# Kernel optimization log

Measured on AMD Instinct MI355X. Metric: run time of the kernel, lower is better.

The kernel has to match this reference:

```python
import jax, jax.numpy as jnp
import numpy as np

BLOCK_SIZE = 1024
OUTLIER_SIGMA = 3.0
OUT_FEATURES = 11008
IN_FEATURES = 4096
TOKENS = 64


def _quantize_mixed_np(W):
    """Faithful numpy port of quantize_mixed (BLOCK_SIZE divides numel exactly here)."""
    flat = W.astype(np.float32).reshape(-1)
    nb = flat.size // BLOCK_SIZE
    blocks = flat.reshape(nb, BLOCK_SIZE)
    mu = blocks.mean(axis=1, keepdims=True)
    sig = np.maximum(blocks.std(axis=1, ddof=1, keepdims=True), 1e-8)  # torch.std is unbiased
    outlier = np.abs(blocks - mu) > OUTLIER_SIGMA * sig
    abs_max = np.maximum(np.abs(np.where(outlier, 0.0, blocks)).max(axis=1), 1e-8)
    scales = (abs_max / 127.0).astype(np.float16)
    q = np.clip(np.round(blocks / abs_max[:, None] * 127.0), -127, 127).astype(np.int8)
    all_pos = np.arange(nb, dtype=np.int64)[:, None] * BLOCK_SIZE + np.arange(BLOCK_SIZE, dtype=np.int64)[None, :]
    int8_data = q[~outlier]                      # row-major == torch order
    fp16_data = blocks[outlier].astype(np.float16)
    int8_pos = all_pos[~outlier].astype(np.int32)
    fp16_pos = all_pos[outlier].astype(np.int32)
    block_idx = np.nonzero(~outlier)[0].astype(np.int32)  # block index per int8 value
    return int8_data, fp16_data, scales, int8_pos, fp16_pos, block_idx


def setup_inputs() -> dict:
    key = jax.random.key(0)
    k_x, k_b = jax.random.split(key)
    rng = np.random.default_rng(0)
    W = (rng.standard_normal((OUT_FEATURES, IN_FEATURES)) * 0.02).astype(np.float32)
    int8_data, fp16_data, scales, int8_pos, fp16_pos, block_idx = _quantize_mixed_np(W)
    x = jax.random.normal(k_x, (TOKENS, IN_FEATURES), dtype=jnp.float16)
    bias = jax.random.normal(k_b, (OUT_FEATURES,), dtype=jnp.float16) * jnp.float16(0.02)
    return {
        "x": x,
        "int8_data": jnp.asarray(int8_data),
        "fp16_data": jnp.asarray(fp16_data),
        "scales": jnp.asarray(scales),
        "bias": bias,
        "int8_pos": jnp.asarray(int8_pos),
        "fp16_pos": jnp.asarray(fp16_pos),
        "block_idx": jnp.asarray(block_idx),
    }


def reference(x, int8_data, fp16_data, scales, bias, int8_pos, fp16_pos, block_idx):
    out_features = bias.shape[0]
    in_features = x.shape[1]
    numel = out_features * in_features  # divisible by BLOCK_SIZE for these dims
    # dequantize_mixed: scatter fp16 outliers and dequantized int8 values into flat fp16 buffer
    flat = jnp.zeros((numel,), dtype=jnp.float16)
    flat = flat.at[fp16_pos].set(fp16_data)
    flat = flat.at[int8_pos].set(int8_data.astype(jnp.float16) * scales[block_idx])
    W = flat.reshape(out_features, in_features)
    # F.linear(x, W, bias) in fp16
    return jnp.dot(x.astype(jnp.float16), W.T) + bias
```

## Files before the change

### kernel.cpp

```cpp
#include <hip/hip_runtime.h>
#include <hip/hip_fp16.h>

#define TOK   64
#define INF   4096
#define OUTF  11008
#define NUMEL (OUTF * INF)
#define NSLC  (NUMEL / 64)
#define NBLK  (OUTF / 16)
#define KSPL  4
#define OUTN  (TOK * OUTF)

typedef __attribute__((ext_vector_type(8))) _Float16 half8;
typedef __attribute__((ext_vector_type(4))) _Float16 half4;
typedef __attribute__((ext_vector_type(4))) float floatx4;
typedef __attribute__((ext_vector_type(4), aligned(4))) int int4u;
typedef __attribute__((ext_vector_type(4))) int int4a;

__global__ __launch_bounds__(256) void precompute_kernel(
    const float* __restrict__ x, const int* __restrict__ fppos, int nf,
    _Float16* __restrict__ x16, int* __restrict__ meta) {
  const int t = blockIdx.x * 256 + threadIdx.x;
  if (t < (TOK * INF) / 4) {
    const floatx4 f = *(const floatx4*)&x[t * 4];
    half4 h;
    h[0] = (_Float16)f[0]; h[1] = (_Float16)f[1];
    h[2] = (_Float16)f[2]; h[3] = (_Float16)f[3];
    *(half4*)&x16[t * 4] = h;
  }
  if (t < NSLC) {
    const int target = t << 6;
    int lo = 0, hi = nf;
    while (lo < hi) {
      const int mid = (lo + hi) >> 1;
      if (fppos[mid] < target) lo = mid + 1; else hi = mid;
    }
    unsigned long long mask = 0ull;
    int j = lo;
    while (j < nf) {
      const int d = fppos[j] - target;
      if (d >= 64) break;
      mask |= 1ull << d;
      ++j;
    }
    int4a mv;
    mv[0] = lo;
    mv[1] = (int)(unsigned)(mask & 0xffffffffu);
    mv[2] = (int)(unsigned)(mask >> 32);
    mv[3] = 0;
    *(int4a*)&meta[t * 4] = mv;
  }
}

__device__ __forceinline__ void meta_window1(const int p0, const int4a mv,
                                             int& i0, unsigned& m8) {
  const unsigned mlo = (unsigned)mv[1];
  const unsigned mhi = (unsigned)mv[2];
  const int off = p0 & 63;
  m8 = 0xffu & (off < 32 ? (mlo >> off) : (mhi >> (off - 32)));
  const unsigned bl = (off >= 32) ? mlo : (mlo & ((1u << off) - 1u));
  const unsigned bh = (off >= 32) ? (mhi & ((1u << (off - 32)) - 1u)) : 0u;
  i0 = p0 - mv[0] - (__popc(bl) + __popc(bh));
}

__device__ __forceinline__ half8 finish_slot(
    const unsigned m8, const int i0, const int p0, const float s,
    const int (&l)[8], const int* __restrict__ i8,
    const float* __restrict__ fpdat, const int n8) {
  const int f = (int)m8;
  float ov[8];
#pragma unroll
  for (int e = 0; e < 8; ++e) ov[e] = 0.f;
  if (f) {
    int fi = p0 - i0;
#pragma unroll
    for (int e = 0; e < 8; ++e) {
      if ((f >> e) & 1) { ov[e] = fpdat[fi]; ++fi; }
    }
  }

  half8 oh;
  if (i0 + 8 <= n8) {
    if (f == 0) {
#pragma unroll
      for (int e = 0; e < 8; ++e) oh[e] = (_Float16)((float)l[e] * s);
    } else {
      int q = 0;
#pragma unroll
      for (int e = 0; e < 8; ++e) {
        const int flg = (f >> e) & 1;
        int lv = l[0];
#pragma unroll
        for (int qq = 1; qq < 8; ++qq) lv = (q == qq) ? l[qq] : lv;
        oh[e] = flg ? (_Float16)ov[e] : (_Float16)((float)lv * s);
        q += 1 - flg;
      }
    }
  } else {
    int c = 0;
    const int m = n8 - 1;
#pragma unroll
    for (int e = 0; e < 8; ++e) {
      const int flg = (f >> e) & 1;
      int idx = i0 + e - c;
      idx = idx < 0 ? 0 : (idx > m ? m : idx);
      oh[e] = flg ? (_Float16)ov[e] : (_Float16)((float)i8[idx] * s);
      c += flg;
    }
  }
  return oh;
}

struct Pre {
  int la[8], lb[8];
  int i0a, i0b;
  unsigned m8a, m8b;
  float va0, va1, vb0, vb1;
  half8 A[8];
};

__global__ __launch_bounds__(256, 3) void gemm_fused(
    const _Float16* __restrict__ x16, const int* __restrict__ i8,
    const float* __restrict__ fpdat, const float* __restrict__ scales,
    const int* __restrict__ meta, float* __restrict__ part,
    const int n8, const int nf) {
  __shared__ float red[4 * 64 * 16];

  const int tid  = threadIdx.x;
  const int wave = tid >> 6;
  const int lane = tid & 63;
  const int quad = lane >> 4;
  const int ln   = lane & 15;
  const int nt   = blockIdx.x >> 2;
  const int kq   = blockIdx.x & 3;
  const int n0   = nt << 4;
  const int kbas = kq * 1024 + wave * 256;
  const int qoff = quad * 8;

  const int prow  = n0 + ln;
  const int pbase = prow * INF + kbas;
  const float s   = scales[prow * 4 + kq];

#define ISSUE(BNK, CC, MV)                                                   \
  do {                                                                       \
    const int p0a_ = pbase + (CC) * 64 + qoff;                               \
    meta_window1(p0a_, (MV), BNK.i0a, BNK.m8a);                              \
    meta_window1(p0a_ + 32, (MV), BNK.i0b, BNK.m8b);                         \
    if (BNK.i0a + 8 <= n8) {                                                 \
      *(int4u*)&BNK.la[0] = *(const int4u*)&i8[BNK.i0a];                     \
      *(int4u*)&BNK.la[4] = *(const int4u*)&i8[BNK.i0a + 4];                 \
    }                                                                        \
    if (BNK.i0b + 8 <= n8) {                                                 \
      *(int4u*)&BNK.lb[0] = *(const int4u*)&i8[BNK.i0b];                     \
      *(int4u*)&BNK.lb[4] = *(const int4u*)&i8[BNK.i0b + 4];                 \
    }                                                                        \
    if (BNK.m8a) {                                                           \
      const int fia_ = p0a_ - BNK.i0a;                                       \
      BNK.va0 = fpdat[fia_];                                                 \
      BNK.va1 = fpdat[fia_ + 1 < nf ? fia_ + 1 : nf - 1];                    \
    }                                                                        \
    if (BNK.m8b) {                                                           \
      const int fib_ = p0a_ + 32 - BNK.i0b;                                  \
      BNK.vb0 = fpdat[fib_];                                                 \
      BNK.vb1 = fpdat[fib_ + 1 < nf ? fib_ + 1 : nf - 1];                    \
    }                                                                        \
    const _Float16* ap_ = &x16[ln * INF + kbas + (CC) * 64 + qoff];          \
    BNK.A[0] = *(const half8*)&ap_[0];                                       \
    BNK.A[1] = *(const half8*)&ap_[16 * INF];                                \
    BNK.A[2] = *(const half8*)&ap_[32 * INF];                                \
    BNK.A[3] = *(const half8*)&ap_[48 * INF];                                \
    BNK.A[4] = *(const half8*)&ap_[32];                                      \
    BNK.A[5] = *(const half8*)&ap_[16 * INF + 32];                           \
    BNK.A[6] = *(const half8*)&ap_[32 * INF + 32];                           \
    BNK.A[7] = *(const half8*)&ap_[48 * INF + 32];                           \
  } while (0)

#define FSLOT(OH, LARR, M8, I0, V0, V1)                                      \
  do {                                                                       \
    const int f_ = (int)(M8);                                                \
    if ((I0) + 8 <= n8) {                                                    \
      if (f_ == 0) {                                                         \
        _Pragma("unroll")                                                    \
        for (int e = 0; e < 8; ++e) OH[e] = (_Float16)((float)LARR[e] * s);  \
      } else {                                                               \
        int q_ = 0;                                                          \
        _Pragma("unroll")                                                    \
        for (int e = 0; e < 8; ++e) {                                        \
          const int flg = (f_ >> e) & 1;                                     \
          const int rank = __popc(f_ & ((1 << e) - 1));                      \
          const float fv = (rank == 0) ? (V0) : (V1);                        \
          int lv = LARR[0];                                                  \
          _Pragma("unroll")                                                  \
          for (int qq = 1; qq < 8; ++qq) lv = (q_ == qq) ? LARR[qq] : lv;    \
          OH[e] = flg ? (_Float16)fv : (_Float16)((float)lv * s);            \
          q_ += 1 - flg;                                                     \
        }                                                                    \
      }                                                                      \
    } else {                                                                 \
      int c_ = 0;                                                            \
      const int m_ = n8 - 1;                                                 \
      _Pragma("unroll")                                                      \
      for (int e = 0; e < 8; ++e) {                                          \
        const int flg = (f_ >> e) & 1;                                       \
        const int rank = __popc(f_ & ((1 << e) - 1));                        \
        const float fv = (rank == 0) ? (V0) : (V1);                          \
        int idx = (I0) + e - c_;                                             \
        idx = idx < 0 ? 0 : (idx > m_ ? m_ : idx);                           \
        OH[e] = flg ? (_Float16)fv : (_Float16)((float)i8[idx] * s);         \
        c_ += flg;                                                           \
      }                                                                      \
    }                                                                        \
  } while (0)

#define FIN_MFMA(BNK, CC)                                                    \
  do {                                                                       \
    const int p0a_ = pbase + (CC) * 64 + qoff;                               \
    half8 b0, b1;                                                            \
    FSLOT(b0, BNK.la, BNK.m8a, BNK.i0a, BNK.va0, BNK.va1);                   \
    FSLOT(b1, BNK.lb, BNK.m8b, BNK.i0b, BNK.vb0, BNK.vb1);                   \
    if (__any(__popc((int)BNK.m8a) > 2 || __popc((int)BNK.m8b) > 2)) {       \
      if (__popc((int)BNK.m8a) > 2)                                          \
        b0 = finish_slot(BNK.m8a, BNK.i0a, p0a_, s, BNK.la, i8, fpdat, n8);  \
      if (__popc((int)BNK.m8b) > 2)                                          \
        b1 = finish_slot(BNK.m8b, BNK.i0b, p0a_ + 32, s, BNK.lb,             \
                         i8, fpdat, n8);                                     \
    }                                                                        \
    acc0 = __builtin_amdgcn_mfma_f32_16x16x32_f16(BNK.A[0], b0, acc0, 0,0,0);\
    acc1 = __builtin_amdgcn_mfma_f32_16x16x32_f16(BNK.A[1], b0, acc1, 0,0,0);\
    acc2 = __builtin_amdgcn_mfma_f32_16x16x32_f16(BNK.A[2], b0, acc2, 0,0,0);\
    acc3 = __builtin_amdgcn_mfma_f32_16x16x32_f16(BNK.A[3], b0, acc3, 0,0,0);\
    acc0 = __builtin_amdgcn_mfma_f32_16x16x32_f16(BNK.A[4], b1, acc0, 0,0,0);\
    acc1 = __builtin_amdgcn_mfma_f32_16x16x32_f16(BNK.A[5], b1, acc1, 0,0,0);\
    acc2 = __builtin_amdgcn_mfma_f32_16x16x32_f16(BNK.A[6], b1, acc2, 0,0,0);\
    acc3 = __builtin_amdgcn_mfma_f32_16x16x32_f16(BNK.A[7], b1, acc3, 0,0,0);\
  } while (0)

  int4a mzA = *(const int4a*)&meta[(pbase >> 6) * 4];
  int4a mzB = *(const int4a*)&meta[((pbase + 64) >> 6) * 4];
  Pre pA, pB;
  ISSUE(pA, 0, mzA);

  floatx4 acc0 = {0,0,0,0}, acc1 = {0,0,0,0}, acc2 = {0,0,0,0}, acc3 = {0,0,0,0};

  ISSUE(pB, 1, mzB);
  mzA = *(const int4a*)&meta[((pbase + 128) >> 6) * 4];
  FIN_MFMA(pA, 0);
  ISSUE(pA, 2, mzA);
  mzB = *(const int4a*)&meta[((pbase + 192) >> 6) * 4];
  FIN_MFMA(pB, 1);
  ISSUE(pB, 3, mzB);
  FIN_MFMA(pA, 2);
  FIN_MFMA(pB, 3);

#undef ISSUE
#undef FSLOT
#undef FIN_MFMA

  const int mb = quad * 4;
#pragma unroll
  for (int i = 0; i < 4; ++i) red[wave * 1024 + (mb + i)      * 16 + ln] = acc0[i];
#pragma unroll
  for (int i = 0; i < 4; ++i) red[wave * 1024 + (16 + mb + i) * 16 + ln] = acc1[i];
#pragma unroll
  for (int i = 0; i < 4; ++i) red[wave * 1024 + (32 + mb + i) * 16 + ln] = acc2[i];
#pragma unroll
  for (int i = 0; i < 4; ++i) red[wave * 1024 + (48 + mb + i) * 16 + ln] = acc3[i];
  __syncthreads();

  float* pp = &part[(size_t)kq * OUTN];
#pragma unroll
  for (int c2 = 0; c2 < 4; ++c2) {
    const int cell = tid + c2 * 256;
    const int mm = cell >> 4, nn = cell & 15;
    pp[mm * OUTF + n0 + nn] =
        red[cell] + red[1024 + cell] + red[2048 + cell] + red[3072 + cell];
  }
}

__global__ __launch_bounds__(256) void reduce_kernel(
    const float* __restrict__ part, const float* __restrict__ bias,
    float* __restrict__ out) {
  const int t  = blockIdx.x * 256 + threadIdx.x;
  const int i4 = t * 4;
  floatx4 a = *(const floatx4*)&part[i4];
#pragma unroll
  for (int k = 1; k < KSPL; ++k) {
    const floatx4 b = *(const floatx4*)&part[(size_t)k * OUTN + i4];
    a[0] += b[0]; a[1] += b[1]; a[2] += b[2]; a[3] += b[3];
  }
  const int nn = i4 % OUTF;
  const floatx4 bb = *(const floatx4*)&bias[nn];
  a[0] += bb[0]; a[1] += bb[1]; a[2] += bb[2]; a[3] += bb[3];
  *(floatx4*)&out[i4] = a;
}

extern "C" void kernel_launch(void* const* d_in, const int* in_sizes, int n_in,
                              void* d_out, int out_size, void* d_ws,
                              size_t ws_size, hipStream_t stream) {
  const float* x      = (const float*)d_in[0];
  const int*   i8     = (const int*)d_in[1];
  const float* fpdat  = (const float*)d_in[2];
  const float* scales = (const float*)d_in[3];
  const float* bias   = (const float*)d_in[4];
  const int*   fppos  = (const int*)d_in[6];

  char* wsp = (char*)d_ws;
  _Float16* x16  = (_Float16*)wsp;
  int*      meta = (int*)(wsp + (size_t)TOK * INF * sizeof(_Float16));
  float*    part = (float*)(wsp + (size_t)TOK * INF * sizeof(_Float16)
                                + (size_t)NSLC * 16);
  float*    out  = (float*)d_out;

  const int n8 = in_sizes[1];
  const int nf = in_sizes[2];

  precompute_kernel<<<NSLC / 256, 256, 0, stream>>>(x, fppos, nf, x16, meta);
  gemm_fused<<<NBLK * KSPL, 256, 0, stream>>>(x16, i8, fpdat, scales, meta,
                                              part, n8, nf);
  reduce_kernel<<<OUTN / (4 * 256), 256, 0, stream>>>(part, bias, out);
}
```

Measured before the change: 438.3 us.

## Seed outlier binary search per chunk and load A fragments just-in-time

A new small kernel binary-searches the outlier position list once per 4096-element chunk. The precompute kernel then narrows each per-slice search to that chunk's range, which cuts global-memory search steps. The GEMM kernel stops prefetching the eight A fragments into the double-buffered Pre struct and loads them inside each stage instead. This lowers register pressure so launch bounds can rise from 3 to 4 blocks per SM, at the cost of less latency hiding for the A loads and one extra kernel launch.

```diff
diff --git a/kernel.cpp b/kernel.cpp
--- a/kernel.cpp
+++ b/kernel.cpp
@@ -6,6 +6,7 @@
 #define OUTF  11008
 #define NUMEL (OUTF * INF)
 #define NSLC  (NUMEL / 64)
+#define NSEED (NSLC / 64)
 #define NBLK  (OUTF / 16)
 #define KSPL  4
 #define OUTN  (TOK * OUTF)
@@ -16,9 +17,24 @@
 typedef __attribute__((ext_vector_type(4), aligned(4))) int int4u;
 typedef __attribute__((ext_vector_type(4))) int int4a;
 
+__global__ __launch_bounds__(256) void seed_kernel(
+    const int* __restrict__ fppos, int nf, int* __restrict__ seed) {
+  const int j = blockIdx.x * 256 + threadIdx.x;
+  if (j <= NSEED) {
+    const int target = j * 4096;
+    int lo = 0, hi = nf;
+    while (lo < hi) {
+      const int mid = (lo + hi) >> 1;
+      if (fppos[mid] < target) lo = mid + 1; else hi = mid;
+    }
+    seed[j] = lo;
+  }
+}
+
 __global__ __launch_bounds__(256) void precompute_kernel(
     const float* __restrict__ x, const int* __restrict__ fppos, int nf,
-    _Float16* __restrict__ x16, int* __restrict__ meta) {
+    const int* __restrict__ seed, _Float16* __restrict__ x16,
+    int* __restrict__ meta) {
   const int t = blockIdx.x * 256 + threadIdx.x;
   if (t < (TOK * INF) / 4) {
     const floatx4 f = *(const floatx4*)&x[t * 4];
@@ -29,7 +45,7 @@
   }
   if (t < NSLC) {
     const int target = t << 6;
-    int lo = 0, hi = nf;
+    int lo = seed[t >> 6], hi = seed[(t >> 6) + 1];
     while (lo < hi) {
       const int mid = (lo + hi) >> 1;
       if (fppos[mid] < target) lo = mid + 1; else hi = mid;
@@ -115,10 +131,9 @@
   int i0a, i0b;
   unsigned m8a, m8b;
   float va0, va1, vb0, vb1;
-  half8 A[8];
 };
 
-__global__ __launch_bounds__(256, 3) void gemm_fused(
+__global__ __launch_bounds__(256, 4) void gemm_fused(
     const _Float16* __restrict__ x16, const int* __restrict__ i8,
     const float* __restrict__ fpdat, const float* __restrict__ scales,
     const int* __restrict__ meta, float* __restrict__ part,
@@ -163,15 +178,6 @@
       BNK.vb0 = fpdat[fib_];                                                 \
       BNK.vb1 = fpdat[fib_ + 1 < nf ? fib_ + 1 : nf - 1];                    \
     }                                                                        \
-    const _Float16* ap_ = &x16[ln * INF + kbas + (CC) * 64 + qoff];          \
-    BNK.A[0] = *(const half8*)&ap_[0];                                       \
-    BNK.A[1] = *(const half8*)&ap_[16 * INF];                                \
-    BNK.A[2] = *(const half8*)&ap_[32 * INF];                                \
-    BNK.A[3] = *(const half8*)&ap_[48 * INF];                                \
-    BNK.A[4] = *(const half8*)&ap_[32];                                      \
-    BNK.A[5] = *(const half8*)&ap_[16 * INF + 32];                           \
-    BNK.A[6] = *(const half8*)&ap_[32 * INF + 32];                           \
-    BNK.A[7] = *(const half8*)&ap_[48 * INF + 32];                           \
   } while (0)
 
 #define FSLOT(OH, LARR, M8, I0, V0, V1)                                      \
@@ -211,6 +217,17 @@
     }                                                                        \
   } while (0)
 
+#define LOADA(CC)                                                            \
+  const _Float16* ap_ = &x16[ln * INF + kbas + (CC) * 64 + qoff];            \
+  const half8 A0 = *(const half8*)&ap_[0];                                   \
+  const half8 A1 = *(const half8*)&ap_[16 * INF];                            \
+  const half8 A2 = *(const half8*)&ap_[32 * INF];                            \
+  const half8 A3 = *(const half8*)&ap_[48 * INF];                            \
+  const half8 A4 = *(const half8*)&ap_[32];                                  \
+  const half8 A5 = *(const half8*)&ap_[16 * INF + 32];                       \
+  const half8 A6 = *(const half8*)&ap_[32 * INF + 32];                       \
+  const half8 A7 = *(const half8*)&ap_[48 * INF + 32]
+
 #define FIN_MFMA(BNK, CC)                                                    \
   do {                                                                       \
     const int p0a_ = pbase + (CC) * 64 + qoff;                               \
@@ -224,14 +241,14 @@
         b1 = finish_slot(BNK.m8b, BNK.i0b, p0a_ + 32, s, BNK.lb,             \
                          i8, fpdat, n8);                                     \
     }                                                                        \
-    acc0 = __builtin_amdgcn_mfma_f32_16x16x32_f16(BNK.A[0], b0, acc0, 0,0,0);\
-    acc1 = __builtin_amdgcn_mfma_f32_16x16x32_f16(BNK.A[1], b0, acc1, 0,0,0);\
-    acc2 = __builtin_amdgcn_mfma_f32_16x16x32_f16(BNK.A[2], b0, acc2, 0,0,0);\
-    acc3 = __builtin_amdgcn_mfma_f32_16x16x32_f16(BNK.A[3], b0, acc3, 0,0,0);\
-    acc0 = __builtin_amdgcn_mfma_f32_16x16x32_f16(BNK.A[4], b1, acc0, 0,0,0);\
-    acc1 = __builtin_amdgcn_mfma_f32_16x16x32_f16(BNK.A[5], b1, acc1, 0,0,0);\
-    acc2 = __builtin_amdgcn_mfma_f32_16x16x32_f16(BNK.A[6], b1, acc2, 0,0,0);\
-    acc3 = __builtin_amdgcn_mfma_f32_16x16x32_f16(BNK.A[7], b1, acc3, 0,0,0);\
+    acc0 = __builtin_amdgcn_mfma_f32_16x16x32_f16(A0, b0, acc0, 0, 0, 0);    \
+    acc1 = __builtin_amdgcn_mfma_f32_16x16x32_f16(A1, b0, acc1, 0, 0, 0);    \
+    acc2 = __builtin_amdgcn_mfma_f32_16x16x32_f16(A2, b0, acc2, 0, 0, 0);    \
+    acc3 = __builtin_amdgcn_mfma_f32_16x16x32_f16(A3, b0, acc3, 0, 0, 0);    \
+    acc0 = __builtin_amdgcn_mfma_f32_16x16x32_f16(A4, b1, acc0, 0, 0, 0);    \
+    acc1 = __builtin_amdgcn_mfma_f32_16x16x32_f16(A5, b1, acc1, 0, 0, 0);    \
+    acc2 = __builtin_amdgcn_mfma_f32_16x16x32_f16(A6, b1, acc2, 0, 0, 0);    \
+    acc3 = __builtin_amdgcn_mfma_f32_16x16x32_f16(A7, b1, acc3, 0, 0, 0);    \
   } while (0)
 
   int4a mzA = *(const int4a*)&meta[(pbase >> 6) * 4];
@@ -241,18 +258,31 @@
 
   floatx4 acc0 = {0,0,0,0}, acc1 = {0,0,0,0}, acc2 = {0,0,0,0}, acc3 = {0,0,0,0};
 
-  ISSUE(pB, 1, mzB);
-  mzA = *(const int4a*)&meta[((pbase + 128) >> 6) * 4];
-  FIN_MFMA(pA, 0);
-  ISSUE(pA, 2, mzA);
-  mzB = *(const int4a*)&meta[((pbase + 192) >> 6) * 4];
-  FIN_MFMA(pB, 1);
-  ISSUE(pB, 3, mzB);
-  FIN_MFMA(pA, 2);
-  FIN_MFMA(pB, 3);
+  {
+    LOADA(0);
+    ISSUE(pB, 1, mzB);
+    mzA = *(const int4a*)&meta[((pbase + 128) >> 6) * 4];
+    FIN_MFMA(pA, 0);
+  }
+  {
+    LOADA(1);
+    ISSUE(pA, 2, mzA);
+    mzB = *(const int4a*)&meta[((pbase + 192) >> 6) * 4];
+    FIN_MFMA(pB, 1);
+  }
+  {
+    LOADA(2);
+    ISSUE(pB, 3, mzB);
+    FIN_MFMA(pA, 2);
+  }
+  {
+    LOADA(3);
+    FIN_MFMA(pB, 3);
+  }
 
 #undef ISSUE
 #undef FSLOT
+#undef LOADA
 #undef FIN_MFMA
 
   const int mb = quad * 4;
@@ -308,12 +338,17 @@
   int*      meta = (int*)(wsp + (size_t)TOK * INF * sizeof(_Float16));
   float*    part = (float*)(wsp + (size_t)TOK * INF * sizeof(_Float16)
                                 + (size_t)NSLC * 16);
+  int*      seed = (int*)(wsp + (size_t)TOK * INF * sizeof(_Float16)
+                              + (size_t)NSLC * 16
+                              + (size_t)KSPL * OUTN * sizeof(float));
   float*    out  = (float*)d_out;
 
   const int n8 = in_sizes[1];
   const int nf = in_sizes[2];
 
-  precompute_kernel<<<NSLC / 256, 256, 0, stream>>>(x, fppos, nf, x16, meta);
+  seed_kernel<<<(NSEED + 256) / 256 + 1, 256, 0, stream>>>(fppos, nf, seed);
+  precompute_kernel<<<NSLC / 256, 256, 0, stream>>>(x, fppos, nf, seed,
+                                                    x16, meta);
   gemm_fused<<<NBLK * KSPL, 256, 0, stream>>>(x16, i8, fpdat, scales, meta,
                                               part, n8, nf);
   reduce_kernel<<<OUTN / (4 * 256), 256, 0, stream>>>(part, bias, out);
```

Measured after the change: 452.7 us. 1.03x slower.

## Split K eight ways, halve per-wave work, and drop A prefetch buffers

Applied to the files above, without the earlier changes.

Raises the K split from 4 to 8, so each wave handles 128 K elements (2 chunks) instead of 256, and the grid doubles in size. The per-bank A registers are replaced by one shared set loaded just before each MFMA group, and the outlier fp32 loads become unconditional with clamped indices. Launch bounds rise to 4 blocks per SIMD to lift occupancy. The aim is more parallelism and lower register pressure. In exchange, partial-sum traffic and the reduction work double, and A-load latency is exposed before the MFMAs with less overlap.

```diff
diff --git a/kernel.cpp b/kernel.cpp
--- a/kernel.cpp
+++ b/kernel.cpp
@@ -7,7 +7,7 @@
 #define NUMEL (OUTF * INF)
 #define NSLC  (NUMEL / 64)
 #define NBLK  (OUTF / 16)
-#define KSPL  4
+#define KSPL  8
 #define OUTN  (TOK * OUTF)
 
 typedef __attribute__((ext_vector_type(8))) _Float16 half8;
@@ -115,10 +115,9 @@
   int i0a, i0b;
   unsigned m8a, m8b;
   float va0, va1, vb0, vb1;
-  half8 A[8];
 };
 
-__global__ __launch_bounds__(256, 3) void gemm_fused(
+__global__ __launch_bounds__(256, 4) void gemm_fused(
     const _Float16* __restrict__ x16, const int* __restrict__ i8,
     const float* __restrict__ fpdat, const float* __restrict__ scales,
     const int* __restrict__ meta, float* __restrict__ part,
@@ -130,15 +129,15 @@
   const int lane = tid & 63;
   const int quad = lane >> 4;
   const int ln   = lane & 15;
-  const int nt   = blockIdx.x >> 2;
-  const int kq   = blockIdx.x & 3;
+  const int nt   = blockIdx.x >> 3;
+  const int kq   = blockIdx.x & 7;
   const int n0   = nt << 4;
-  const int kbas = kq * 1024 + wave * 256;
+  const int kbas = kq * 512 + wave * 128;
   const int qoff = quad * 8;
 
   const int prow  = n0 + ln;
   const int pbase = prow * INF + kbas;
-  const float s   = scales[prow * 4 + kq];
+  const float s   = scales[prow * 4 + (kq >> 1)];
 
 #define ISSUE(BNK, CC, MV)                                                   \
   do {                                                                       \
@@ -153,25 +152,17 @@
       *(int4u*)&BNK.lb[0] = *(const int4u*)&i8[BNK.i0b];                     \
       *(int4u*)&BNK.lb[4] = *(const int4u*)&i8[BNK.i0b + 4];                 \
     }                                                                        \
-    if (BNK.m8a) {                                                           \
-      const int fia_ = p0a_ - BNK.i0a;                                       \
+      \
+    {                                                                        \
+      int fia_ = p0a_ - BNK.i0a;                                             \
+      fia_ = fia_ < nf - 1 ? fia_ : nf - 1;                                  \
       BNK.va0 = fpdat[fia_];                                                 \
       BNK.va1 = fpdat[fia_ + 1 < nf ? fia_ + 1 : nf - 1];                    \
-    }                                                                        \
-    if (BNK.m8b) {                                                           \
-      const int fib_ = p0a_ + 32 - BNK.i0b;                                  \
+      int fib_ = p0a_ + 32 - BNK.i0b;                                        \
+      fib_ = fib_ < nf - 1 ? fib_ : nf - 1;                                  \
       BNK.vb0 = fpdat[fib_];                                                 \
       BNK.vb1 = fpdat[fib_ + 1 < nf ? fib_ + 1 : nf - 1];                    \
     }                                                                        \
-    const _Float16* ap_ = &x16[ln * INF + kbas + (CC) * 64 + qoff];          \
-    BNK.A[0] = *(const half8*)&ap_[0];                                       \
-    BNK.A[1] = *(const half8*)&ap_[16 * INF];                                \
-    BNK.A[2] = *(const half8*)&ap_[32 * INF];                                \
-    BNK.A[3] = *(const half8*)&ap_[48 * INF];                                \
-    BNK.A[4] = *(const half8*)&ap_[32];                                      \
-    BNK.A[5] = *(const half8*)&ap_[16 * INF + 32];                           \
-    BNK.A[6] = *(const half8*)&ap_[32 * INF + 32];                           \
-    BNK.A[7] = *(const half8*)&ap_[48 * INF + 32];                           \
   } while (0)
 
 #define FSLOT(OH, LARR, M8, I0, V0, V1)                                      \
@@ -211,6 +202,19 @@
     }                                                                        \
   } while (0)
 
+#define LOADA(CC)                                                            \
+  do {                                                                       \
+    const _Float16* ap_ = &x16[ln * INF + kbas + (CC) * 64 + qoff];          \
+    A0 = *(const half8*)&ap_[0];                                             \
+    A1 = *(const half8*)&ap_[16 * INF];                                      \
+    A2 = *(const half8*)&ap_[32 * INF];                                      \
+    A3 = *(const half8*)&ap_[48 * INF];                                      \
+    A4 = *(const half8*)&ap_[32];                                            \
+    A5 = *(const half8*)&ap_[16 * INF + 32];                                 \
+    A6 = *(const half8*)&ap_[32 * INF + 32];                                 \
+    A7 = *(const half8*)&ap_[48 * INF + 32];                                 \
+  } while (0)
+
 #define FIN_MFMA(BNK, CC)                                                    \
   do {                                                                       \
     const int p0a_ = pbase + (CC) * 64 + qoff;                               \
@@ -224,35 +228,33 @@
         b1 = finish_slot(BNK.m8b, BNK.i0b, p0a_ + 32, s, BNK.lb,             \
                          i8, fpdat, n8);                                     \
     }                                                                        \
-    acc0 = __builtin_amdgcn_mfma_f32_16x16x32_f16(BNK.A[0], b0, acc0, 0,0,0);\
-    acc1 = __builtin_amdgcn_mfma_f32_16x16x32_f16(BNK.A[1], b0, acc1, 0,0,0);\
-    acc2 = __builtin_amdgcn_mfma_f32_16x16x32_f16(BNK.A[2], b0, acc2, 0,0,0);\
-    acc3 = __builtin_amdgcn_mfma_f32_16x16x32_f16(BNK.A[3], b0, acc3, 0,0,0);\
-    acc0 = __builtin_amdgcn_mfma_f32_16x16x32_f16(BNK.A[4], b1, acc0, 0,0,0);\
-    acc1 = __builtin_amdgcn_mfma_f32_16x16x32_f16(BNK.A[5], b1, acc1, 0,0,0);\
-    acc2 = __builtin_amdgcn_mfma_f32_16x16x32_f16(BNK.A[6], b1, acc2, 0,0,0);\
-    acc3 = __builtin_amdgcn_mfma_f32_16x16x32_f16(BNK.A[7], b1, acc3, 0,0,0);\
+    acc0 = __builtin_amdgcn_mfma_f32_16x16x32_f16(A0, b0, acc0, 0, 0, 0);    \
+    acc1 = __builtin_amdgcn_mfma_f32_16x16x32_f16(A1, b0, acc1, 0, 0, 0);    \
+    acc2 = __builtin_amdgcn_mfma_f32_16x16x32_f16(A2, b0, acc2, 0, 0, 0);    \
+    acc3 = __builtin_amdgcn_mfma_f32_16x16x32_f16(A3, b0, acc3, 0, 0, 0);    \
+    acc0 = __builtin_amdgcn_mfma_f32_16x16x32_f16(A4, b1, acc0, 0, 0, 0);    \
+    acc1 = __builtin_amdgcn_mfma_f32_16x16x32_f16(A5, b1, acc1, 0, 0, 0);    \
+    acc2 = __builtin_amdgcn_mfma_f32_16x16x32_f16(A6, b1, acc2, 0, 0, 0);    \
+    acc3 = __builtin_amdgcn_mfma_f32_16x16x32_f16(A7, b1, acc3, 0, 0, 0);    \
   } while (0)
 
-  int4a mzA = *(const int4a*)&meta[(pbase >> 6) * 4];
-  int4a mzB = *(const int4a*)&meta[((pbase + 64) >> 6) * 4];
+  const int4a mz0 = *(const int4a*)&meta[(pbase >> 6) * 4];
+  const int4a mz1 = *(const int4a*)&meta[((pbase + 64) >> 6) * 4];
+  half8 A0, A1, A2, A3, A4, A5, A6, A7;
+  LOADA(0);
   Pre pA, pB;
-  ISSUE(pA, 0, mzA);
+  ISSUE(pA, 0, mz0);
+  ISSUE(pB, 1, mz1);
 
   floatx4 acc0 = {0,0,0,0}, acc1 = {0,0,0,0}, acc2 = {0,0,0,0}, acc3 = {0,0,0,0};
 
-  ISSUE(pB, 1, mzB);
-  mzA = *(const int4a*)&meta[((pbase + 128) >> 6) * 4];
   FIN_MFMA(pA, 0);
-  ISSUE(pA, 2, mzA);
-  mzB = *(const int4a*)&meta[((pbase + 192) >> 6) * 4];
+  LOADA(1);
   FIN_MFMA(pB, 1);
-  ISSUE(pB, 3, mzB);
-  FIN_MFMA(pA, 2);
-  FIN_MFMA(pB, 3);
 
 #undef ISSUE
 #undef FSLOT
+#undef LOADA
 #undef FIN_MFMA
 
   const int mb = quad * 4;
```

New measurement: 435.2 us. About the same (-0.7%).
